# Performance work log

Hardware: AMD Instinct MI355X
Metric: run time of the kernel (lower is better)

The kernel has to match this reference:

```python
import jax, jax.numpy as jnp
import numpy as np

N, E = 50000, 640000          # nodes, edges
F_IN, HID, CLS = 128, 128, 64  # feature dims


def setup_inputs() -> dict:
    key = jax.random.key(0)
    ks = jax.random.split(key, 12)
    x = jax.random.normal(ks[0], (N, F_IN), dtype=jnp.float32)
    edge_index = jax.random.randint(ks[1], (2, E), 0, N, dtype=jnp.int32)
    s_in = 1.0 / np.sqrt(F_IN)
    s_h = 1.0 / np.sqrt(HID)
    return {
        "x": x,
        "edge_index": edge_index,
        "W0": jax.random.normal(ks[2], (F_IN, HID), jnp.float32) * s_in,
        "b0": jnp.zeros((HID,), jnp.float32),
        "W1": jax.random.normal(ks[3], (HID, HID), jnp.float32) * s_h,
        "b1": jnp.zeros((HID,), jnp.float32),
        "W2": jax.random.normal(ks[4], (HID, HID), jnp.float32) * s_h,
        "b2": jnp.zeros((HID,), jnp.float32),
        "W_lin": jax.random.normal(ks[5], (HID, CLS), jnp.float32) * s_h,
        "b_lin": jnp.zeros((CLS,), jnp.float32),
    }


def reference(x, edge_index, W0, b0, W1, b1, W2, b2, W_lin, b_lin):
    # GCNConv (PyG defaults): out = D^-1/2 (A + I) D^-1/2 (x @ W) + b
    row, col = edge_index[0], edge_index[1]  # source -> target
    # degree with self-loop (graph is fixed across layers, compute norms once)
    deg = jnp.zeros((N,), x.dtype).at[col].add(1.0) + 1.0
    dinv = jax.lax.rsqrt(deg)                 # deg >= 1, safe
    enorm = (dinv[row] * dinv[col])[:, None]  # [E,1] edge norm
    snorm = (dinv * dinv)[:, None]            # [N,1] self-loop norm

    def conv(h, W, b):
        h = h @ W                                             # [N,HID]
        agg = jnp.zeros_like(h).at[col].add(h[row] * enorm)   # neighbor agg
        return agg + h * snorm + b                            # + self loop + bias

    h = jax.nn.relu(conv(x, W0, b0))
    h = jax.nn.relu(conv(h, W1, b1))
    h = jax.nn.relu(conv(h, W2, b2))
    return h @ W_lin + b_lin
```

## Files before the change

### kernel.cpp

```cpp
#include <hip/hip_runtime.h>
#include <hip/hip_fp16.h>

#define N_NODES 50000
#define HID 128
#define CLS 64

#define NBINS 196
#define NBLK 256
#define LBUF_CAP 4096
#define WTOT 57344
#define GEMM0_BLOCKS 782
#define AROW 136

typedef __attribute__((ext_vector_type(8))) _Float16 f16x8;
typedef __attribute__((ext_vector_type(4))) float f32x4;

__global__ __launch_bounds__(256) void hist_wsplit_kernel(
    const int* __restrict__ col, int* __restrict__ hist,
    const float* __restrict__ W0, const float* __restrict__ W1,
    const float* __restrict__ W2, const float* __restrict__ Wl,
    __half* __restrict__ o0h, __half* __restrict__ o0l,
    __half* __restrict__ o1h, __half* __restrict__ o1l,
    __half* __restrict__ o2h, __half* __restrict__ o2l,
    __half* __restrict__ o3h, __half* __restrict__ o3l,
    int E, int chunk) {
    int widx = blockIdx.x * 256 + threadIdx.x;
    if (widx < WTOT) {
        const float* W;
        __half *oh, *ol;
        int NCdim, local;
        if (widx < 16384)      { W = W0; oh = o0h; ol = o0l; NCdim = 128; local = widx; }
        else if (widx < 32768) { W = W1; oh = o1h; ol = o1l; NCdim = 128; local = widx - 16384; }
        else if (widx < 49152) { W = W2; oh = o2h; ol = o2l; NCdim = 128; local = widx - 32768; }
        else                   { W = Wl; oh = o3h; ol = o3l; NCdim = 64;  local = widx - 49152; }
        int nn = local >> 7;
        int k = local & 127;
        float v = W[(size_t)k * NCdim + nn];
        __half h = __float2half_rn(v);
        oh[local] = h;
        ol[local] = __float2half_rn(v - __half2float(h));
    }
    __shared__ int h[NBINS];
    for (int i = threadIdx.x; i < NBINS; i += 256) h[i] = 0;
    __syncthreads();
    int b = blockIdx.x;
    int beg = b * chunk;
    int end = min(E, beg + chunk);
    if (beg < end) {
        int vend = beg + ((end - beg) & ~3);
        for (int i = beg + threadIdx.x * 4; i < vend; i += 1024) {
            int4 c4 = *(const int4*)(col + i);
            atomicAdd(&h[c4.x >> 8], 1);
            atomicAdd(&h[c4.y >> 8], 1);
            atomicAdd(&h[c4.z >> 8], 1);
            atomicAdd(&h[c4.w >> 8], 1);
        }
        int i = vend + threadIdx.x;
        if (i < end) atomicAdd(&h[col[i] >> 8], 1);
    }
    __syncthreads();
    for (int i = threadIdx.x; i < NBINS; i += 256)
        hist[i * NBLK + b] = h[i];
}

__global__ __launch_bounds__(256) void scatter_kernel(
    const int* __restrict__ row, const int* __restrict__ col,
    const int* __restrict__ hist, int* __restrict__ binBase_g,
    int* __restrict__ sbuf_src, unsigned char* __restrict__ sbuf_c,
    int E, int chunk) {
    __shared__ int sTot[256];
    __shared__ int cur[NBINS];
    int b = blockIdx.x, t = threadIdx.x;
    int partial = 0, total = 0;
    if (t < NBINS) {
        const int4* r4 = (const int4*)(hist + t * NBLK);
        int nb4 = b >> 2, rem = b & 3;
        for (int j = 0; j < NBLK / 4; ++j) {
            int4 v = r4[j];
            int s = v.x + v.y + v.z + v.w;
            total += s;
            if (j < nb4) partial += s;
            else if (j == nb4) {
                if (rem > 0) partial += v.x;
                if (rem > 1) partial += v.y;
                if (rem > 2) partial += v.z;
            }
        }
    }
    sTot[t] = (t < NBINS) ? total : 0;
    __syncthreads();
#pragma unroll
    for (int off = 1; off < 256; off <<= 1) {
        int u = (t >= off) ? sTot[t - off] : 0;
        __syncthreads();
        sTot[t] += u;
        __syncthreads();
    }
    int myBase = sTot[t] - total;
    if (t < NBINS) cur[t] = myBase + partial;
    if (b == 0) {
        if (t < NBINS) binBase_g[t] = myBase;
        if (t == 0) binBase_g[NBINS] = E;
    }
    __syncthreads();
    int beg = b * chunk;
    int end = min(E, beg + chunk);
    if (beg >= end) return;
    int vend = beg + ((end - beg) & ~3);
    for (int i = beg + t * 4; i < vend; i += 1024) {
        int4 c4 = *(const int4*)(col + i);
        int4 r4 = *(const int4*)(row + i);
        int p;
        p = atomicAdd(&cur[c4.x >> 8], 1); sbuf_src[p] = r4.x; sbuf_c[p] = (unsigned char)(c4.x & 255);
        p = atomicAdd(&cur[c4.y >> 8], 1); sbuf_src[p] = r4.y; sbuf_c[p] = (unsigned char)(c4.y & 255);
        p = atomicAdd(&cur[c4.z >> 8], 1); sbuf_src[p] = r4.z; sbuf_c[p] = (unsigned char)(c4.z & 255);
        p = atomicAdd(&cur[c4.w >> 8], 1); sbuf_src[p] = r4.w; sbuf_c[p] = (unsigned char)(c4.w & 255);
    }
    int i = vend + t;
    if (i < end) {
        int c = col[i];
        int p = atomicAdd(&cur[c >> 8], 1);
        sbuf_src[p] = row[i];
        sbuf_c[p] = (unsigned char)(c & 255);
    }
}

__device__ __forceinline__ void gemm0_body(
    const float* __restrict__ x, const __half* __restrict__ Bh,
    const __half* __restrict__ Bl, __half* __restrict__ C, int M, int rowTile) {
    constexpr int NT = 8;
    int lane = threadIdx.x & 63;
    int m0 = rowTile << 4;
    if (m0 >= M) return;
    int mr = lane & 15;
    int kq = (lane >> 4) << 3;

    const float*  af = x + (size_t)(m0 + mr) * 128 + kq;
    const __half* bh = Bh + (size_t)mr * 128 + kq;
    const __half* bl = Bl + (size_t)mr * 128 + kq;

    f32x4 acc[NT];
#pragma unroll
    for (int t = 0; t < NT; ++t) acc[t] = (f32x4){0.f, 0.f, 0.f, 0.f};
#pragma unroll
    for (int kc = 0; kc < 128; kc += 32) {
        float4 lo = *(const float4*)(af + kc);
        float4 hi = *(const float4*)(af + kc + 4);
        f16x8 a;
        a[0] = (_Float16)lo.x; a[1] = (_Float16)lo.y;
        a[2] = (_Float16)lo.z; a[3] = (_Float16)lo.w;
        a[4] = (_Float16)hi.x; a[5] = (_Float16)hi.y;
        a[6] = (_Float16)hi.z; a[7] = (_Float16)hi.w;
#pragma unroll
        for (int t = 0; t < NT; ++t) {
            f16x8 wh = *(const f16x8*)(bh + (size_t)t * 16 * 128 + kc);
            f16x8 wl = *(const f16x8*)(bl + (size_t)t * 16 * 128 + kc);
            acc[t] = __builtin_amdgcn_mfma_f32_16x16x32_f16(a, wh, acc[t], 0, 0, 0);
            acc[t] = __builtin_amdgcn_mfma_f32_16x16x32_f16(a, wl, acc[t], 0, 0, 0);
        }
    }
    int r0 = m0 + ((lane >> 4) << 2);
    int cc = lane & 15;
#pragma unroll
    for (int t = 0; t < NT; ++t)
#pragma unroll
        for (int r = 0; r < 4; ++r)
            C[(size_t)(r0 + r) * 128 + t * 16 + cc] =
                __float2half_rn(acc[t][r]);
}

__global__ __launch_bounds__(256) void csrplace_gemm0_kernel(
    const int* __restrict__ binBase,
    const int* __restrict__ sbuf_src, const unsigned char* __restrict__ sbuf_c,
    float* __restrict__ dinv, int* __restrict__ row_ptr, int* __restrict__ csr_src,
    const float* __restrict__ x, const __half* __restrict__ W0h,
    const __half* __restrict__ W0l, __half* __restrict__ h2, int n, int E) {
    __shared__ int lcnt[256];
    __shared__ int lcur[256];
    __shared__ int ss[256];
    __shared__ int lbuf[LBUF_CAP];
    int b = blockIdx.x;
    if (b >= NBINS) {
        gemm0_body(x, W0h, W0l, h2, n, (b - NBINS) * 4 + (threadIdx.x >> 6));
        return;
    }
    int t = threadIdx.x;
    lcnt[t] = 0;
    __syncthreads();
    int beg = binBase[b], end = binBase[b + 1];
    for (int j = beg + t; j < end; j += 256)
        atomicAdd(&lcnt[sbuf_c[j]], 1);
    __syncthreads();
    int deg = lcnt[t];
    int node = b * 256 + t;
    if (node < n) dinv[node] = rsqrtf((float)deg + 1.0f);
    ss[t] = deg;
    __syncthreads();
#pragma unroll
    for (int off = 1; off < 256; off <<= 1) {
        int u = (t >= off) ? ss[t - off] : 0;
        __syncthreads();
        ss[t] += u;
        __syncthreads();
    }
    int excl = ss[t] - deg;
    lcur[t] = excl;
    int total = ss[255];
    if (node < n) row_ptr[node] = beg + excl;
    if (b == 0 && t == 0) row_ptr[n] = E;
    __syncthreads();
    for (int j = beg + t; j < end; j += 256) {
        int c = sbuf_c[j];
        int pos = atomicAdd(&lcur[c], 1);
        lbuf[pos] = sbuf_src[j];
    }
    __syncthreads();
    for (int j = t; j < total; j += 256) csr_src[beg + j] = lbuf[j];
}

template<int NC, bool HEAD>
__global__ __launch_bounds__(256) void agg_gemm_kernel(
    const __half* __restrict__ h2, const int* __restrict__ row_ptr,
    const int* __restrict__ csr_src, const float* __restrict__ dinv,
    const float* __restrict__ bias,
    const __half* __restrict__ Bh, const __half* __restrict__ Bl,
    const float* __restrict__ gbias, void* __restrict__ Cv, int n) {
    __shared__ __half Als[16][AROW];
    int wave = threadIdx.x >> 6;
    int lane = threadIdx.x & 63;
    int m0 = blockIdx.x << 4;

    int g = lane >> 4;
    int l16 = lane & 15;
    int baseLane = lane & 48;
    int lr = (wave << 2) + g;
    int wid = m0 + lr;
    const __half* hrow = h2 + (l16 << 3);

    if (wid < n) {
        int beg = row_ptr[wid];
        int end = row_ptr[wid + 1];
        float dv = dinv[wid];
        float acc[8];
#pragma unroll
        for (int i = 0; i < 8; ++i) acc[i] = 0.f;

        for (int base = beg; base < end; base += 16) {
            int cnt = end - base;
            if (cnt > 16) cnt = 16;
            int msrc = 0;
            float mw = 0.f;
            if (l16 < cnt) {
                msrc = csr_src[base + l16];
                mw = dinv[msrc] * dv;
            }
            int j = 0;
            for (; j + 4 <= cnt; j += 4) {
                int s0 = __shfl(msrc, baseLane + j);
                int s1 = __shfl(msrc, baseLane + j + 1);
                int s2 = __shfl(msrc, baseLane + j + 2);
                int s3 = __shfl(msrc, baseLane + j + 3);
                float w0 = __shfl(mw, baseLane + j);
                float w1 = __shfl(mw, baseLane + j + 1);
                float w2 = __shfl(mw, baseLane + j + 2);
                float w3 = __shfl(mw, baseLane + j + 3);
                f16x8 v0 = *(const f16x8*)(hrow + ((size_t)s0 << 7));
                f16x8 v1 = *(const f16x8*)(hrow + ((size_t)s1 << 7));
                f16x8 v2 = *(const f16x8*)(hrow + ((size_t)s2 << 7));
                f16x8 v3 = *(const f16x8*)(hrow + ((size_t)s3 << 7));
#pragma unroll
                for (int i = 0; i < 8; ++i) {
                    acc[i] = fmaf((float)v0[i], w0, acc[i]);
                    acc[i] = fmaf((float)v1[i], w1, acc[i]);
                    acc[i] = fmaf((float)v2[i], w2, acc[i]);
                    acc[i] = fmaf((float)v3[i], w3, acc[i]);
                }
            }
            for (; j + 2 <= cnt; j += 2) {
                int s0 = __shfl(msrc, baseLane + j);
                int s1 = __shfl(msrc, baseLane + j + 1);
                float w0 = __shfl(mw, baseLane + j);
                float w1 = __shfl(mw, baseLane + j + 1);
                f16x8 v0 = *(const f16x8*)(hrow + ((size_t)s0 << 7));
                f16x8 v1 = *(const f16x8*)(hrow + ((size_t)s1 << 7));
#pragma unroll
                for (int i = 0; i < 8; ++i) {
                    acc[i] = fmaf((float)v0[i], w0, acc[i]);
                    acc[i] = fmaf((float)v1[i], w1, acc[i]);
                }
            }
            if (j < cnt) {
                int s0 = __shfl(msrc, baseLane + j);
                float w0 = __shfl(mw, baseLane + j);
                f16x8 v0 = *(const f16x8*)(hrow + ((size_t)s0 << 7));
#pragma unroll
                for (int i = 0; i < 8; ++i)
                    acc[i] = fmaf((float)v0[i], w0, acc[i]);
            }
        }
        float sn = dv * dv;
        f16x8 sv = *(const f16x8*)(hrow + ((size_t)wid << 7));
        float4 ba = *(const float4*)(bias + (l16 << 3));
        float4 bb = *(const float4*)(bias + (l16 << 3) + 4);
        float o[8];
#pragma unroll
        for (int i = 0; i < 8; ++i) o[i] = fmaf((float)sv[i], sn, acc[i]);
        o[0] += ba.x; o[1] += ba.y; o[2] += ba.z; o[3] += ba.w;
        o[4] += bb.x; o[5] += bb.y; o[6] += bb.z; o[7] += bb.w;
        f16x8 pk;
#pragma unroll
        for (int i = 0; i < 8; ++i) pk[i] = (_Float16)fmaxf(o[i], 0.f);
        *(f16x8*)&Als[lr][l16 << 3] = pk;
    }
    __syncthreads();

    constexpr int NT = NC / 16;
    constexpr int TPW = NT / 4;
    int mr = lane & 15;
    int kq = (lane >> 4) << 3;
    const __half* bh = Bh + (size_t)mr * 128 + kq;
    const __half* bl = Bl + (size_t)mr * 128 + kq;

    f32x4 acc[TPW];
#pragma unroll
    for (int t = 0; t < TPW; ++t) acc[t] = (f32x4){0.f, 0.f, 0.f, 0.f};
#pragma unroll
    for (int kc = 0; kc < 128; kc += 32) {
        f16x8 a = *(const f16x8*)&Als[mr][kq + kc];
#pragma unroll
        for (int t = 0; t < TPW; ++t) {
            int tile = wave * TPW + t;
            f16x8 wh = *(const f16x8*)(bh + (size_t)tile * 16 * 128 + kc);
            f16x8 wl = *(const f16x8*)(bl + (size_t)tile * 16 * 128 + kc);
            acc[t] = __builtin_amdgcn_mfma_f32_16x16x32_f16(a, wh, acc[t], 0, 0, 0);
            acc[t] = __builtin_amdgcn_mfma_f32_16x16x32_f16(a, wl, acc[t], 0, 0, 0);
        }
    }
    int r0 = m0 + ((lane >> 4) << 2);
    int cc = lane & 15;
#pragma unroll
    for (int t = 0; t < TPW; ++t) {
        int tile = wave * TPW + t;
        float bsv = HEAD ? gbias[tile * 16 + cc] : 0.f;
#pragma unroll
        for (int r = 0; r < 4; ++r) {
            if (r0 + r >= n) break;
            size_t idx = (size_t)(r0 + r) * NC + tile * 16 + cc;
            float val = acc[t][r] + bsv;
            if (HEAD)
                ((float*)Cv)[idx] = val;
            else
                ((__half*)Cv)[idx] = __float2half_rn(val);
        }
    }
}

extern "C" void kernel_launch(void* const* d_in, const int* in_sizes, int n_in,
                              void* d_out, int out_size, void* d_ws, size_t ws_size,
                              hipStream_t stream) {
    const float* x  = (const float*)d_in[0];
    const int* ei   = (const int*)d_in[1];
    const float* W0 = (const float*)d_in[2];
    const float* b0 = (const float*)d_in[3];
    const float* W1 = (const float*)d_in[4];
    const float* b1 = (const float*)d_in[5];
    const float* W2 = (const float*)d_in[6];
    const float* b2 = (const float*)d_in[7];
    const float* Wl = (const float*)d_in[8];
    const float* bl = (const float*)d_in[9];
    float* out = (float*)d_out;

    const int N = N_NODES;
    const int E = in_sizes[1] / 2;
    const int* row = ei;
    const int* col = ei + E;
    const int chunk = (((E + NBLK - 1) / NBLK) + 3) & ~3;

    char* ws = (char*)d_ws;
    auto alloc = [&](size_t bytes) {
        char* p = ws;
        ws += (bytes + 255) & ~(size_t)255;
        return p;
    };
    int*   hist    = (int*)alloc((size_t)NBINS * NBLK * 4);
    int*   binBase = (int*)alloc((size_t)(NBINS + 1) * 4);
    int*   sbuf_src= (int*)alloc((size_t)E * 4);
    unsigned char* sbuf_c = (unsigned char*)alloc((size_t)E);
    int*   row_ptr = (int*)alloc((size_t)(N + 1) * 4);
    float* dinv    = (float*)alloc((size_t)N * 4);
    int*   csr_src = (int*)alloc((size_t)E * 4);
    __half* h2a    = (__half*)alloc((size_t)N * HID * 2);
    __half* h2b    = (__half*)alloc((size_t)N * HID * 2);
    __half* Wt_h[4];
    __half* Wt_l[4];
    for (int i = 0; i < 3; ++i) {
        Wt_h[i] = (__half*)alloc((size_t)HID * HID * 2);
        Wt_l[i] = (__half*)alloc((size_t)HID * HID * 2);
    }
    Wt_h[3] = (__half*)alloc((size_t)CLS * HID * 2);
    Wt_l[3] = (__half*)alloc((size_t)CLS * HID * 2);

    hist_wsplit_kernel<<<NBLK, 256, 0, stream>>>(col, hist, W0, W1, W2, Wl,
        Wt_h[0], Wt_l[0], Wt_h[1], Wt_l[1], Wt_h[2], Wt_l[2], Wt_h[3], Wt_l[3], E, chunk);
    scatter_kernel<<<NBLK, 256, 0, stream>>>(row, col, hist, binBase, sbuf_src, sbuf_c, E, chunk);
    csrplace_gemm0_kernel<<<NBINS + GEMM0_BLOCKS, 256, 0, stream>>>(
        binBase, sbuf_src, sbuf_c, dinv, row_ptr, csr_src,
        x, Wt_h[0], Wt_l[0], h2a, N, E);

    const int fusedBlocks = (N + 15) / 16;

    agg_gemm_kernel<128, false><<<fusedBlocks, 256, 0, stream>>>(
        h2a, row_ptr, csr_src, dinv, b0, Wt_h[1], Wt_l[1], nullptr, h2b, N);
    agg_gemm_kernel<128, false><<<fusedBlocks, 256, 0, stream>>>(
        h2b, row_ptr, csr_src, dinv, b1, Wt_h[2], Wt_l[2], nullptr, h2a, N);
    agg_gemm_kernel<64, true><<<fusedBlocks, 256, 0, stream>>>(
        h2a, row_ptr, csr_src, dinv, b2, Wt_h[3], Wt_l[3], bl, out, N);
}
```

Before: 268.9 us.

## Split fused aggregate+GEMM into column-sliced aggregation and separate MFMA GEMM kernels

Replaces the fused per-layer aggregation+GEMM kernel with two kernels. The first is a gather kernel in which each block handles one 32-column slice of 16 nodes using half2 loads and 8-way unrolled neighbor fetches. The second is a standalone MFMA GEMM that works in place, with each wave computing all output tiles for 16 rows. CSR source indices shrink to 16-bit to halve index traffic, and nontemporal stores are used for intermediates. This adds three extra launches and an extra round trip of activations through memory. The 16-bit indices only hold because N is 50000.

Result: slower. 393.6 us (+46.3%).

```diff
diff --git a/kernel.cpp b/kernel.cpp
--- a/kernel.cpp
+++ b/kernel.cpp
@@ -10,7 +10,8 @@
 #define LBUF_CAP 4096
 #define WTOT 57344
 #define GEMM0_BLOCKS 782
-#define AROW 136
+#define AGG_BLOCKS 12500
+#define GEMMF_BLOCKS 782
 
 typedef __attribute__((ext_vector_type(8))) _Float16 f16x8;
 typedef __attribute__((ext_vector_type(4))) float f32x4;
@@ -172,7 +173,8 @@
 __global__ __launch_bounds__(256) void csrplace_gemm0_kernel(
     const int* __restrict__ binBase,
     const int* __restrict__ sbuf_src, const unsigned char* __restrict__ sbuf_c,
-    float* __restrict__ dinv, int* __restrict__ row_ptr, int* __restrict__ csr_src,
+    float* __restrict__ dinv, int* __restrict__ row_ptr,
+    unsigned short* __restrict__ csr_src,
     const float* __restrict__ x, const __half* __restrict__ W0h,
     const __half* __restrict__ W0l, __half* __restrict__ h2, int n, int E) {
     __shared__ int lcnt[256];
@@ -215,142 +217,116 @@
         lbuf[pos] = sbuf_src[j];
     }
     __syncthreads();
-    for (int j = t; j < total; j += 256) csr_src[beg + j] = lbuf[j];
+    for (int j = t; j < total; j += 256)
+        csr_src[beg + j] = (unsigned short)lbuf[j];
+}
+
+__global__ __launch_bounds__(256) void agg_slice_kernel(
+    const __half* __restrict__ h2, const int* __restrict__ row_ptr,
+    const unsigned short* __restrict__ csr_src, const float* __restrict__ dinv,
+    const float* __restrict__ bias, __half* __restrict__ hout, int n) {
+    int b = blockIdx.x;
+    int s = b & 3;
+    int tile = b >> 2;
+    int t = threadIdx.x;
+    int grp = t >> 4;
+    int l16 = t & 15;
+    int wid = tile * 16 + grp;
+    if (wid >= n) return;
+    int cOff = (s << 5) + (l16 << 1);
+    int hvo = (s << 4) + l16;
+    const __half2* hv = (const __half2*)h2;
+
+    int base = row_ptr[wid];
+    int deg = row_ptr[wid + 1] - base;
+    float dv = dinv[wid];
+    float ax = 0.f, ay = 0.f;
+
+    for (int j0 = 0; j0 < deg; j0 += 8) {
+        int sidx[8];
+#pragma unroll
+        for (int p = 0; p < 8; ++p) {
+            int jj = j0 + p;
+            sidx[p] = csr_src[base + (jj < deg ? jj : deg - 1)];
+        }
+        float wv[8];
+#pragma unroll
+        for (int p = 0; p < 8; ++p)
+            wv[p] = (j0 + p < deg) ? dinv[sidx[p]] * dv : 0.f;
+        __half2 r[8];
+#pragma unroll
+        for (int p = 0; p < 8; ++p)
+            r[p] = hv[((size_t)sidx[p] << 6) + hvo];
+#pragma unroll
+        for (int p = 0; p < 8; ++p) {
+            float2 v = __half22float2(r[p]);
+            ax = fmaf(v.x, wv[p], ax);
+            ay = fmaf(v.y, wv[p], ay);
+        }
+    }
+    float sn = dv * dv;
+    float2 self = __half22float2(hv[((size_t)wid << 6) + hvo]);
+    float2 bb = *(const float2*)(bias + cOff);
+    float ox = fmaxf(fmaf(self.x, sn, ax) + bb.x, 0.f);
+    float oy = fmaxf(fmaf(self.y, sn, ay) + bb.y, 0.f);
+    __half2 pk = __float22half2_rn(make_float2(ox, oy));
+    unsigned int pkbits;
+    __builtin_memcpy(&pkbits, &pk, 4);
+    __builtin_nontemporal_store(pkbits,
+                                (unsigned int*)hout + ((size_t)wid << 6) + hvo);
 }
 
 template<int NC, bool HEAD>
-__global__ __launch_bounds__(256) void agg_gemm_kernel(
-    const __half* __restrict__ h2, const int* __restrict__ row_ptr,
-    const int* __restrict__ csr_src, const float* __restrict__ dinv,
-    const float* __restrict__ bias,
-    const __half* __restrict__ Bh, const __half* __restrict__ Bl,
-    const float* __restrict__ gbias, void* __restrict__ Cv, int n) {
-    __shared__ __half Als[16][AROW];
+__global__ __launch_bounds__(256) void gemm_f16_kernel(
+    const __half* A, const __half* __restrict__ Bh, const __half* __restrict__ Bl,
+    const float* __restrict__ gbias, void* Cv, int n) {
+    constexpr int NT = NC / 16;
     int wave = threadIdx.x >> 6;
     int lane = threadIdx.x & 63;
-    int m0 = blockIdx.x << 4;
-
-    int g = lane >> 4;
-    int l16 = lane & 15;
-    int baseLane = lane & 48;
-    int lr = (wave << 2) + g;
-    int wid = m0 + lr;
-    const __half* hrow = h2 + (l16 << 3);
-
-    if (wid < n) {
-        int beg = row_ptr[wid];
-        int end = row_ptr[wid + 1];
-        float dv = dinv[wid];
-        float acc[8];
-#pragma unroll
-        for (int i = 0; i < 8; ++i) acc[i] = 0.f;
-
-        for (int base = beg; base < end; base += 16) {
-            int cnt = end - base;
-            if (cnt > 16) cnt = 16;
-            int msrc = 0;
-            float mw = 0.f;
-            if (l16 < cnt) {
-                msrc = csr_src[base + l16];
-                mw = dinv[msrc] * dv;
-            }
-            int j = 0;
-            for (; j + 4 <= cnt; j += 4) {
-                int s0 = __shfl(msrc, baseLane + j);
-                int s1 = __shfl(msrc, baseLane + j + 1);
-                int s2 = __shfl(msrc, baseLane + j + 2);
-                int s3 = __shfl(msrc, baseLane + j + 3);
-                float w0 = __shfl(mw, baseLane + j);
-                float w1 = __shfl(mw, baseLane + j + 1);
-                float w2 = __shfl(mw, baseLane + j + 2);
-                float w3 = __shfl(mw, baseLane + j + 3);
-                f16x8 v0 = *(const f16x8*)(hrow + ((size_t)s0 << 7));
-                f16x8 v1 = *(const f16x8*)(hrow + ((size_t)s1 << 7));
-                f16x8 v2 = *(const f16x8*)(hrow + ((size_t)s2 << 7));
-                f16x8 v3 = *(const f16x8*)(hrow + ((size_t)s3 << 7));
-#pragma unroll
-                for (int i = 0; i < 8; ++i) {
-                    acc[i] = fmaf((float)v0[i], w0, acc[i]);
-                    acc[i] = fmaf((float)v1[i], w1, acc[i]);
-                    acc[i] = fmaf((float)v2[i], w2, acc[i]);
-                    acc[i] = fmaf((float)v3[i], w3, acc[i]);
-                }
-            }
-            for (; j + 2 <= cnt; j += 2) {
-                int s0 = __shfl(msrc, baseLane + j);
-                int s1 = __shfl(msrc, baseLane + j + 1);
-                float w0 = __shfl(mw, baseLane + j);
-                float w1 = __shfl(mw, baseLane + j + 1);
-                f16x8 v0 = *(const f16x8*)(hrow + ((size_t)s0 << 7));
-                f16x8 v1 = *(const f16x8*)(hrow + ((size_t)s1 << 7));
-#pragma unroll
-                for (int i = 0; i < 8; ++i) {
-                    acc[i] = fmaf((float)v0[i], w0, acc[i]);
-                    acc[i] = fmaf((float)v1[i], w1, acc[i]);
-                }
-            }
-            if (j < cnt) {
-                int s0 = __shfl(msrc, baseLane + j);
-                float w0 = __shfl(mw, baseLane + j);
-                f16x8 v0 = *(const f16x8*)(hrow + ((size_t)s0 << 7));
-#pragma unroll
-                for (int i = 0; i < 8; ++i)
-                    acc[i] = fmaf((float)v0[i], w0, acc[i]);
-            }
-        }
-        float sn = dv * dv;
-        f16x8 sv = *(const f16x8*)(hrow + ((size_t)wid << 7));
-        float4 ba = *(const float4*)(bias + (l16 << 3));
-        float4 bb = *(const float4*)(bias + (l16 << 3) + 4);
-        float o[8];
-#pragma unroll
-        for (int i = 0; i < 8; ++i) o[i] = fmaf((float)sv[i], sn, acc[i]);
-        o[0] += ba.x; o[1] += ba.y; o[2] += ba.z; o[3] += ba.w;
-        o[4] += bb.x; o[5] += bb.y; o[6] += bb.z; o[7] += bb.w;
-        f16x8 pk;
-#pragma unroll
-        for (int i = 0; i < 8; ++i) pk[i] = (_Float16)fmaxf(o[i], 0.f);
-        *(f16x8*)&Als[lr][l16 << 3] = pk;
-    }
-    __syncthreads();
-
-    constexpr int NT = NC / 16;
-    constexpr int TPW = NT / 4;
+    int m0 = (blockIdx.x * 4 + wave) << 4;
+    if (m0 >= n) return;
     int mr = lane & 15;
     int kq = (lane >> 4) << 3;
+
+    f16x8 a[4];
+#pragma unroll
+    for (int kc = 0; kc < 4; ++kc)
+        a[kc] = *(const f16x8*)(A + (size_t)(m0 + mr) * 128 + kq + kc * 32);
+
     const __half* bh = Bh + (size_t)mr * 128 + kq;
     const __half* bl = Bl + (size_t)mr * 128 + kq;
 
-    f32x4 acc[TPW];
-#pragma unroll
-    for (int t = 0; t < TPW; ++t) acc[t] = (f32x4){0.f, 0.f, 0.f, 0.f};
-#pragma unroll
-    for (int kc = 0; kc < 128; kc += 32) {
-        f16x8 a = *(const f16x8*)&Als[mr][kq + kc];
-#pragma unroll
-        for (int t = 0; t < TPW; ++t) {
-            int tile = wave * TPW + t;
-            f16x8 wh = *(const f16x8*)(bh + (size_t)tile * 16 * 128 + kc);
-            f16x8 wl = *(const f16x8*)(bl + (size_t)tile * 16 * 128 + kc);
-            acc[t] = __builtin_amdgcn_mfma_f32_16x16x32_f16(a, wh, acc[t], 0, 0, 0);
-            acc[t] = __builtin_amdgcn_mfma_f32_16x16x32_f16(a, wl, acc[t], 0, 0, 0);
+    f32x4 acc[NT];
+#pragma unroll
+    for (int t = 0; t < NT; ++t) acc[t] = (f32x4){0.f, 0.f, 0.f, 0.f};
+#pragma unroll
+    for (int kc = 0; kc < 4; ++kc) {
+#pragma unroll
+        for (int t = 0; t < NT; ++t) {
+            f16x8 wh = *(const f16x8*)(bh + (size_t)t * 16 * 128 + kc * 32);
+            f16x8 wl = *(const f16x8*)(bl + (size_t)t * 16 * 128 + kc * 32);
+            acc[t] = __builtin_amdgcn_mfma_f32_16x16x32_f16(a[kc], wh, acc[t], 0, 0, 0);
+            acc[t] = __builtin_amdgcn_mfma_f32_16x16x32_f16(a[kc], wl, acc[t], 0, 0, 0);
         }
     }
     int r0 = m0 + ((lane >> 4) << 2);
     int cc = lane & 15;
 #pragma unroll
-    for (int t = 0; t < TPW; ++t) {
-        int tile = wave * TPW + t;
-        float bsv = HEAD ? gbias[tile * 16 + cc] : 0.f;
+    for (int t = 0; t < NT; ++t) {
+        float bsv = HEAD ? gbias[t * 16 + cc] : 0.f;
 #pragma unroll
         for (int r = 0; r < 4; ++r) {
             if (r0 + r >= n) break;
-            size_t idx = (size_t)(r0 + r) * NC + tile * 16 + cc;
+            size_t idx = (size_t)(r0 + r) * NC + t * 16 + cc;
             float val = acc[t][r] + bsv;
-            if (HEAD)
+            if (HEAD) {
                 ((float*)Cv)[idx] = val;
-            else
-                ((__half*)Cv)[idx] = __float2half_rn(val);
+            } else {
+                __half hv = __float2half_rn(val);
+                unsigned short hb;
+                __builtin_memcpy(&hb, &hv, 2);
+                __builtin_nontemporal_store(hb, (unsigned short*)Cv + idx);
+            }
         }
     }
 }
@@ -388,7 +364,7 @@
     unsigned char* sbuf_c = (unsigned char*)alloc((size_t)E);
     int*   row_ptr = (int*)alloc((size_t)(N + 1) * 4);
     float* dinv    = (float*)alloc((size_t)N * 4);
-    int*   csr_src = (int*)alloc((size_t)E * 4);
+    unsigned short* csr_src = (unsigned short*)alloc((size_t)E * 2);
     __half* h2a    = (__half*)alloc((size_t)N * HID * 2);
     __half* h2b    = (__half*)alloc((size_t)N * HID * 2);
     __half* Wt_h[4];
@@ -407,12 +383,16 @@
         binBase, sbuf_src, sbuf_c, dinv, row_ptr, csr_src,
         x, Wt_h[0], Wt_l[0], h2a, N, E);
 
-    const int fusedBlocks = (N + 15) / 16;
-
-    agg_gemm_kernel<128, false><<<fusedBlocks, 256, 0, stream>>>(
-        h2a, row_ptr, csr_src, dinv, b0, Wt_h[1], Wt_l[1], nullptr, h2b, N);
-    agg_gemm_kernel<128, false><<<fusedBlocks, 256, 0, stream>>>(
-        h2b, row_ptr, csr_src, dinv, b1, Wt_h[2], Wt_l[2], nullptr, h2a, N);
-    agg_gemm_kernel<64, true><<<fusedBlocks, 256, 0, stream>>>(
-        h2a, row_ptr, csr_src, dinv, b2, Wt_h[3], Wt_l[3], bl, out, N);
-}
+    agg_slice_kernel<<<AGG_BLOCKS, 256, 0, stream>>>(
+        h2a, row_ptr, csr_src, dinv, b0, h2b, N);
+    gemm_f16_kernel<128, false><<<GEMMF_BLOCKS, 256, 0, stream>>>(
+        h2b, Wt_h[1], Wt_l[1], nullptr, h2b, N);
+    agg_slice_kernel<<<AGG_BLOCKS, 256, 0, stream>>>(
+        h2b, row_ptr, csr_src, dinv, b1, h2a, N);
+    gemm_f16_kernel<128, false><<<GEMMF_BLOCKS, 256, 0, stream>>>(
+        h2a, Wt_h[2], Wt_l[2], nullptr, h2a, N);
+    agg_slice_kernel<<<AGG_BLOCKS, 256, 0, stream>>>(
+        h2a, row_ptr, csr_src, dinv, b2, h2b, N);
+    gemm_f16_kernel<64, true><<<GEMMF_BLOCKS, 256, 0, stream>>>(
+        h2b, Wt_h[3], Wt_l[3], bl, out, N);
+}
```

## Split histogram scan into own kernel and store edge sources as 16-bit

Applied to the files above, without the earlier changes.

The histogram prefix scan moves out of scatter_kernel into a new binscan_kernel. Before, every scatter block re-read the whole per-bin histogram to work out its own offsets; now that work is done once per bin. Edge source indices in the staging buffer and the CSR array are narrowed from int to unsigned short, which halves the index bytes written during CSR build and read by each of the three aggregation layers. This costs one extra kernel launch and relies on the node count fitting in 16 bits.

New measurement: 265.5 us (median of 2 runs). Within noise of the previous version (-1.3%).

```diff
diff --git a/kernel.cpp b/kernel.cpp
--- a/kernel.cpp
+++ b/kernel.cpp
@@ -63,41 +63,46 @@
         hist[i * NBLK + b] = h[i];
 }
 
+__global__ __launch_bounds__(256) void binscan_kernel(
+    const int* __restrict__ hist, int* __restrict__ cursorBase,
+    int* __restrict__ binTotal) {
+    __shared__ int ss[256];
+    int bin = blockIdx.x, t = threadIdx.x;
+    int v = hist[bin * NBLK + t];
+    ss[t] = v;
+    __syncthreads();
+#pragma unroll
+    for (int off = 1; off < 256; off <<= 1) {
+        int u = (t >= off) ? ss[t - off] : 0;
+        __syncthreads();
+        ss[t] += u;
+        __syncthreads();
+    }
+    cursorBase[bin * NBLK + t] = ss[t] - v;
+    if (t == 255) binTotal[bin] = ss[255];
+}
+
 __global__ __launch_bounds__(256) void scatter_kernel(
     const int* __restrict__ row, const int* __restrict__ col,
-    const int* __restrict__ hist, int* __restrict__ binBase_g,
-    int* __restrict__ sbuf_src, unsigned char* __restrict__ sbuf_c,
+    const int* __restrict__ binTotal, const int* __restrict__ cursorBase,
+    int* __restrict__ binBase_g,
+    unsigned short* __restrict__ sbuf_src, unsigned char* __restrict__ sbuf_c,
     int E, int chunk) {
-    __shared__ int sTot[256];
+    __shared__ int ss[256];
     __shared__ int cur[NBINS];
     int b = blockIdx.x, t = threadIdx.x;
-    int partial = 0, total = 0;
-    if (t < NBINS) {
-        const int4* r4 = (const int4*)(hist + t * NBLK);
-        int nb4 = b >> 2, rem = b & 3;
-        for (int j = 0; j < NBLK / 4; ++j) {
-            int4 v = r4[j];
-            int s = v.x + v.y + v.z + v.w;
-            total += s;
-            if (j < nb4) partial += s;
-            else if (j == nb4) {
-                if (rem > 0) partial += v.x;
-                if (rem > 1) partial += v.y;
-                if (rem > 2) partial += v.z;
-            }
-        }
-    }
-    sTot[t] = (t < NBINS) ? total : 0;
+    int v = (t < NBINS) ? binTotal[t] : 0;
+    ss[t] = v;
     __syncthreads();
 #pragma unroll
     for (int off = 1; off < 256; off <<= 1) {
-        int u = (t >= off) ? sTot[t - off] : 0;
-        __syncthreads();
-        sTot[t] += u;
-        __syncthreads();
-    }
-    int myBase = sTot[t] - total;
-    if (t < NBINS) cur[t] = myBase + partial;
+        int u = (t >= off) ? ss[t - off] : 0;
+        __syncthreads();
+        ss[t] += u;
+        __syncthreads();
+    }
+    int myBase = ss[t] - v;
+    if (t < NBINS) cur[t] = myBase + cursorBase[t * NBLK + b];
     if (b == 0) {
         if (t < NBINS) binBase_g[t] = myBase;
         if (t == 0) binBase_g[NBINS] = E;
@@ -111,16 +116,16 @@
         int4 c4 = *(const int4*)(col + i);
         int4 r4 = *(const int4*)(row + i);
         int p;
-        p = atomicAdd(&cur[c4.x >> 8], 1); sbuf_src[p] = r4.x; sbuf_c[p] = (unsigned char)(c4.x & 255);
-        p = atomicAdd(&cur[c4.y >> 8], 1); sbuf_src[p] = r4.y; sbuf_c[p] = (unsigned char)(c4.y & 255);
-        p = atomicAdd(&cur[c4.z >> 8], 1); sbuf_src[p] = r4.z; sbuf_c[p] = (unsigned char)(c4.z & 255);
-        p = atomicAdd(&cur[c4.w >> 8], 1); sbuf_src[p] = r4.w; sbuf_c[p] = (unsigned char)(c4.w & 255);
+        p = atomicAdd(&cur[c4.x >> 8], 1); sbuf_src[p] = (unsigned short)r4.x; sbuf_c[p] = (unsigned char)(c4.x & 255);
+        p = atomicAdd(&cur[c4.y >> 8], 1); sbuf_src[p] = (unsigned short)r4.y; sbuf_c[p] = (unsigned char)(c4.y & 255);
+        p = atomicAdd(&cur[c4.z >> 8], 1); sbuf_src[p] = (unsigned short)r4.z; sbuf_c[p] = (unsigned char)(c4.z & 255);
+        p = atomicAdd(&cur[c4.w >> 8], 1); sbuf_src[p] = (unsigned short)r4.w; sbuf_c[p] = (unsigned char)(c4.w & 255);
     }
     int i = vend + t;
     if (i < end) {
         int c = col[i];
         int p = atomicAdd(&cur[c >> 8], 1);
-        sbuf_src[p] = row[i];
+        sbuf_src[p] = (unsigned short)row[i];
         sbuf_c[p] = (unsigned char)(c & 255);
     }
 }
@@ -171,8 +176,9 @@
 
 __global__ __launch_bounds__(256) void csrplace_gemm0_kernel(
     const int* __restrict__ binBase,
-    const int* __restrict__ sbuf_src, const unsigned char* __restrict__ sbuf_c,
-    float* __restrict__ dinv, int* __restrict__ row_ptr, int* __restrict__ csr_src,
+    const unsigned short* __restrict__ sbuf_src, const unsigned char* __restrict__ sbuf_c,
+    float* __restrict__ dinv, int* __restrict__ row_ptr,
+    unsigned short* __restrict__ csr_src,
     const float* __restrict__ x, const __half* __restrict__ W0h,
     const __half* __restrict__ W0l, __half* __restrict__ h2, int n, int E) {
     __shared__ int lcnt[256];
@@ -215,13 +221,14 @@
         lbuf[pos] = sbuf_src[j];
     }
     __syncthreads();
-    for (int j = t; j < total; j += 256) csr_src[beg + j] = lbuf[j];
+    for (int j = t; j < total; j += 256)
+        csr_src[beg + j] = (unsigned short)lbuf[j];
 }
 
 template<int NC, bool HEAD>
 __global__ __launch_bounds__(256) void agg_gemm_kernel(
     const __half* __restrict__ h2, const int* __restrict__ row_ptr,
-    const int* __restrict__ csr_src, const float* __restrict__ dinv,
+    const unsigned short* __restrict__ csr_src, const float* __restrict__ dinv,
     const float* __restrict__ bias,
     const __half* __restrict__ Bh, const __half* __restrict__ Bl,
     const float* __restrict__ gbias, void* __restrict__ Cv, int n) {
@@ -382,13 +389,15 @@
         ws += (bytes + 255) & ~(size_t)255;
         return p;
     };
-    int*   hist    = (int*)alloc((size_t)NBINS * NBLK * 4);
-    int*   binBase = (int*)alloc((size_t)(NBINS + 1) * 4);
-    int*   sbuf_src= (int*)alloc((size_t)E * 4);
-    unsigned char* sbuf_c = (unsigned char*)alloc((size_t)E);
+    int*   hist      = (int*)alloc((size_t)NBINS * NBLK * 4);
+    int*   cursorBase= (int*)alloc((size_t)NBINS * NBLK * 4);
+    int*   binTotal  = (int*)alloc((size_t)NBINS * 4);
+    int*   binBase   = (int*)alloc((size_t)(NBINS + 1) * 4);
+    unsigned short* sbuf_src = (unsigned short*)alloc((size_t)E * 2);
+    unsigned char*  sbuf_c   = (unsigned char*)alloc((size_t)E);
     int*   row_ptr = (int*)alloc((size_t)(N + 1) * 4);
     float* dinv    = (float*)alloc((size_t)N * 4);
-    int*   csr_src = (int*)alloc((size_t)E * 4);
+    unsigned short* csr_src = (unsigned short*)alloc((size_t)E * 2);
     __half* h2a    = (__half*)alloc((size_t)N * HID * 2);
     __half* h2b    = (__half*)alloc((size_t)N * HID * 2);
     __half* Wt_h[4];
@@ -402,7 +411,9 @@
 
     hist_wsplit_kernel<<<NBLK, 256, 0, stream>>>(col, hist, W0, W1, W2, Wl,
         Wt_h[0], Wt_l[0], Wt_h[1], Wt_l[1], Wt_h[2], Wt_l[2], Wt_h[3], Wt_l[3], E, chunk);
-    scatter_kernel<<<NBLK, 256, 0, stream>>>(row, col, hist, binBase, sbuf_src, sbuf_c, E, chunk);
+    binscan_kernel<<<NBINS, 256, 0, stream>>>(hist, cursorBase, binTotal);
+    scatter_kernel<<<NBLK, 256, 0, stream>>>(row, col, binTotal, cursorBase,
+        binBase, sbuf_src, sbuf_c, E, chunk);
     csrplace_gemm0_kernel<<<NBINS + GEMM0_BLOCKS, 256, 0, stream>>>(
         binBase, sbuf_src, sbuf_c, dinv, row_ptr, csr_src,
         x, Wt_h[0], Wt_l[0], h2a, N, E);
```
